# Kernel tuning notes

Measured on AMD Instinct MI355X. Metric: run time of the kernel, lower is better.

Reference implementation:

```python
import jax, jax.numpy as jnp
import numpy as np

B, T, E, H = 2, 2048, 1024, 16
D = E // H  # head_dim = 64


def setup_inputs() -> dict:
    key = jax.random.key(0)
    ks = jax.random.split(key, 9)
    s = 0.02
    x = jax.random.normal(ks[0], (B, T, E), dtype=jnp.float32)
    # additive causal mask, broadcastable to (B, H, T, T)
    causal = jnp.tril(jnp.ones((T, T), dtype=bool))
    uni_causal_mask = jnp.where(causal, 0.0, -1e9).astype(jnp.float32)[None, None]
    # torch Linear weights are (out_features, in_features); out = H*D, in = D
    Wq = jax.random.normal(ks[1], (H * D, D), dtype=jnp.float32) * s
    bq = jax.random.normal(ks[2], (H * D,), dtype=jnp.float32) * s
    Wk = jax.random.normal(ks[3], (H * D, D), dtype=jnp.float32) * s
    bk = jax.random.normal(ks[4], (H * D,), dtype=jnp.float32) * s
    Wv = jax.random.normal(ks[5], (H * D, D), dtype=jnp.float32) * s
    bv = jax.random.normal(ks[6], (H * D,), dtype=jnp.float32) * s
    Wp = jax.random.normal(ks[7], (E, E), dtype=jnp.float32) * s
    bp = jax.random.normal(ks[8], (E,), dtype=jnp.float32) * s
    return {"x": x, "uni_causal_mask": uni_causal_mask,
            "Wq": Wq, "bq": bq, "Wk": Wk, "bk": bk,
            "Wv": Wv, "bv": bv, "Wp": Wp, "bp": bp}


def _per_head_proj(xh, W, b):
    # xh: (B, T, H, D). Original code projects each head's D-dim slice with
    # Linear(D, H*D) and get_head_dim keeps only the diagonal block i for
    # head i, i.e. each head uses W[i*D:(i+1)*D, :] and b[i*D:(i+1)*D].
    W3 = W.reshape(H, D, D)  # (H, out D, in D)
    b2 = b.reshape(H, D)
    y = jnp.einsum('bthi,hoi->bhto', xh, W3) + b2[None, :, None, :]
    return y  # (B, H, T, D)


def reference(x, uni_causal_mask, Wq, bq, Wk, bk, Wv, bv, Wp, bp):
    b, t, e = x.shape
    xh = x.reshape(b, t, H, D)
    q = _per_head_proj(xh, Wq, bq)  # (B,H,T,D)
    k = _per_head_proj(xh, Wk, bk)
    v = _per_head_proj(xh, Wv, bv)
    scale = D ** (-0.5)
    attn = jnp.einsum('bhtd,bhsd->bhts', (q * scale).astype(jnp.float32),
                      k.astype(jnp.float32))
    attn = attn + uni_causal_mask
    attn = jax.nn.softmax(attn, axis=-1).astype(x.dtype)
    out = jnp.einsum('bhts,bhsd->bhtd', attn, v)
    out = out.transpose(0, 2, 1, 3).reshape(b, t, e)
    return out @ Wp.T + bp
```

## Files before the change

### kernel.cpp

```cpp
#include <hip/hip_runtime.h>

typedef __attribute__((ext_vector_type(4))) float f32x4;
typedef __attribute__((ext_vector_type(8))) __bf16 bf16x8;
typedef __attribute__((ext_vector_type(4))) unsigned short us4;
typedef __attribute__((ext_vector_type(8))) unsigned short us8;

#define DEVI static __device__ __forceinline__

constexpr int T_ = 2048, E_ = 1024, H_ = 16, D_ = 64;
#define QSCALE (0.125f * 1.44269504088896f)

DEVI unsigned short f2b(float f) {
  union { __bf16 b; unsigned short u; } c; c.b = (__bf16)f; return c.u;
}

#if __has_builtin(__builtin_amdgcn_exp2f)
DEVI float fexp2(float x) { return __builtin_amdgcn_exp2f(x); }
#else
DEVI float fexp2(float x) { return __expf(x * 0.69314718056f); }
#endif

DEVI f32x4 mfma16(bf16x8 a, bf16x8 b, f32x4 c) {
  return __builtin_amdgcn_mfma_f32_16x16x32_bf16(a, b, c, 0, 0, 0);
}

__launch_bounds__(256)
__global__ void wcvt_kernel(const float* __restrict__ Wq,
                            const float* __restrict__ Wk,
                            const float* __restrict__ Wv,
                            unsigned short* __restrict__ wqb,
                            unsigned short* __restrict__ wkb,
                            unsigned short* __restrict__ wvb)
{
  int blk = blockIdx.x;
  const float* src; unsigned short* dst; float s = 1.0f;
  if (blk < 64)       { src = Wq; dst = wqb; s = QSCALE; }
  else if (blk < 128) { src = Wk; dst = wkb; blk -= 64; }
  else                { src = Wv; dst = wvb; blk -= 128; }
  int i = blk * 256 + threadIdx.x;
  float4 v = *(const float4*)(src + (size_t)i * 4);
  us4 o; o[0] = f2b(v.x * s); o[1] = f2b(v.y * s); o[2] = f2b(v.z * s); o[3] = f2b(v.w * s);
  *(us4*)(dst + (size_t)i * 4) = o;
}

__launch_bounds__(256)
__global__ void wpcvt_kernel(const float* __restrict__ Wp,
                             unsigned short* __restrict__ wpb)
{
  int i = blockIdx.x * 256 + threadIdx.x;
  float4 v = *(const float4*)(Wp + (size_t)i * 4);
  us4 o; o[0] = f2b(v.x); o[1] = f2b(v.y); o[2] = f2b(v.z); o[3] = f2b(v.w);
  *(us4*)(wpb + (size_t)i * 4) = o;
}

__launch_bounds__(256)
__global__ void qkv_kernel(const float* __restrict__ x,
                           const unsigned short* __restrict__ wqb,
                           const float* __restrict__ bq,
                           const unsigned short* __restrict__ wkb,
                           const float* __restrict__ bk,
                           const unsigned short* __restrict__ wvb,
                           const float* __restrict__ bv,
                           unsigned short* __restrict__ qo,
                           unsigned short* __restrict__ ko,
                           unsigned short* __restrict__ vto)
{
  const int bh = blockIdx.x;
  const int b  = bh >> 4;
  const int h  = bh & (H_ - 1);
  const int t0 = blockIdx.y * 128;
  __shared__ unsigned short Xl[128][72];
  __shared__ unsigned short Wl[3][64][72];
  const int tid = threadIdx.x;

  #pragma unroll
  for (int p = 0; p < 8; ++p) {
    int idx = p * 256 + tid;
    int row = idx >> 4, c4 = idx & 15;
    float4 v = *(const float4*)(x + ((size_t)(b * T_ + t0 + row)) * E_ + h * 64 + c4 * 4);
    us4 o; o[0] = f2b(v.x); o[1] = f2b(v.y); o[2] = f2b(v.z); o[3] = f2b(v.w);
    *(us4*)&Xl[row][c4 * 4] = o;
  }
  {
    const unsigned short* wsrc0 = wqb + (size_t)h * 4096;
    const unsigned short* wsrc1 = wkb + (size_t)h * 4096;
    const unsigned short* wsrc2 = wvb + (size_t)h * 4096;
    #pragma unroll
    for (int p = 0; p < 2; ++p) {
      int idx = p * 256 + tid;
      int row = idx >> 3, c8 = (idx & 7) * 8;
      *(us8*)&Wl[0][row][c8] = *(const us8*)(wsrc0 + row * 64 + c8);
      *(us8*)&Wl[1][row][c8] = *(const us8*)(wsrc1 + row * 64 + c8);
      *(us8*)&Wl[2][row][c8] = *(const us8*)(wsrc2 + row * 64 + c8);
    }
  }
  __syncthreads();

  const int w = tid >> 6, lane = tid & 63, lo = lane & 15, g = lane >> 4;
  const int tl0 = w * 32;

  bf16x8 xb[2][2];
  #pragma unroll
  for (int tt = 0; tt < 2; ++tt)
    #pragma unroll
    for (int kd = 0; kd < 2; ++kd)
      xb[tt][kd] = *(const bf16x8*)&Xl[tl0 + tt * 16 + lo][kd * 32 + g * 8];

  #pragma unroll
  for (int tsel = 0; tsel < 2; ++tsel) {
    const float* bias = tsel ? bk : bq;
    unsigned short* outp = tsel ? ko : qo;
    const float bs = tsel ? 1.0f : QSCALE;
    #pragma unroll
    for (int ot = 0; ot < 4; ++ot) {
      bf16x8 a0 = *(const bf16x8*)&Wl[tsel][ot * 16 + lo][g * 8];
      bf16x8 a1 = *(const bf16x8*)&Wl[tsel][ot * 16 + lo][32 + g * 8];
      float4 bv4 = *(const float4*)(bias + h * 64 + ot * 16 + g * 4);
      float bb[4] = {bv4.x * bs, bv4.y * bs, bv4.z * bs, bv4.w * bs};
      #pragma unroll
      for (int tt = 0; tt < 2; ++tt) {
        f32x4 acc = {0.f, 0.f, 0.f, 0.f};
        acc = mfma16(a0, xb[tt][0], acc);
        acc = mfma16(a1, xb[tt][1], acc);
        int tg = t0 + tl0 + tt * 16 + lo;
        us4 pk;
        #pragma unroll
        for (int r = 0; r < 4; ++r) pk[r] = f2b(acc[r] + bb[r]);
        *(us4*)(outp + ((size_t)(bh * T_ + tg)) * 64 + ot * 16 + g * 4) = pk;
      }
    }
  }

  #pragma unroll
  for (int rt = 0; rt < 2; ++rt) {
    bf16x8 a0 = *(const bf16x8*)&Xl[tl0 + rt * 16 + lo][g * 8];
    bf16x8 a1 = *(const bf16x8*)&Xl[tl0 + rt * 16 + lo][32 + g * 8];
    #pragma unroll
    for (int ct = 0; ct < 4; ++ct) {
      bf16x8 b0 = *(const bf16x8*)&Wl[2][ct * 16 + lo][g * 8];
      bf16x8 b1 = *(const bf16x8*)&Wl[2][ct * 16 + lo][32 + g * 8];
      f32x4 acc = {0.f, 0.f, 0.f, 0.f};
      acc = mfma16(a0, b0, acc);
      acc = mfma16(a1, b1, acc);
      int d = ct * 16 + lo;
      float bvs = bv[h * 64 + d];
      int tg = t0 + tl0 + rt * 16 + g * 4;
      us4 pk;
      #pragma unroll
      for (int r = 0; r < 4; ++r) pk[r] = f2b(acc[r] + bvs);
      *(us4*)(vto + ((size_t)(bh * 64 + d)) * T_ + tg) = pk;
    }
  }
}

__launch_bounds__(256)
__global__ void flash_kernel(const unsigned short* __restrict__ q,
                             const unsigned short* __restrict__ kk_,
                             const unsigned short* __restrict__ vt,
                             unsigned short* __restrict__ ao)
{
  const int bh = blockIdx.x;
  const int b = bh >> 4, h = bh & 15;
  const int qt = 31 - blockIdx.y;
  const int t0 = qt * 64;
  __shared__ unsigned short Kl[2][64][64];
  __shared__ unsigned short Vl[3][64][64];
  __shared__ unsigned short Pl[4][16][64];
  const int tid = threadIdx.x, w = tid >> 6, lane = tid & 63, lo = lane & 15, g = lane >> 4;
  const int rs = lo & 7;

  const int srow = tid >> 3, sgi = tid & 7;
  const int sgis = (sgi ^ (srow & 7)) * 8;
  const unsigned short* kbase = kk_ + ((size_t)bh * T_ + srow) * 64 + sgi * 8;
  const unsigned short* vbase = vt + ((size_t)(bh * 64 + srow)) * T_ + sgi * 8;

  const int tw = t0 + w * 16;

  bf16x8 qf[2];
  const unsigned short* qb = q + ((size_t)(bh * T_ + tw + lo)) * 64;
  #pragma unroll
  for (int kd = 0; kd < 2; ++kd)
    qf[kd] = *(const bf16x8*)(qb + kd * 32 + g * 8);

  float m_ = -1e30f, l_ = 0.f;
  f32x4 zero4 = {0.f, 0.f, 0.f, 0.f};
  f32x4 oacc[4];
  #pragma unroll
  for (int dt = 0; dt < 4; ++dt) oacc[dt] = zero4;

  const int nsteps = qt + 1;
  us8 kr0 = *(const us8*)(kbase);
  us8 kr1 = *(const us8*)(kbase + 2048);
  us8 vr0 = *(const us8*)(vbase);
  us8 vr1 = *(const us8*)(vbase + (size_t)32 * T_);
  *(us8*)&Kl[0][srow][sgis] = kr0;
  *(us8*)&Kl[0][srow + 32][sgis] = kr1;
  *(us8*)&Vl[0][srow][sgis] = vr0;
  *(us8*)&Vl[0][srow + 32][sgis] = vr1;
  if (nsteps > 1) {
    kr0 = *(const us8*)(kbase + 4096);
    kr1 = *(const us8*)(kbase + 4096 + 2048);
    vr0 = *(const us8*)(vbase + 64);
    vr1 = *(const us8*)(vbase + 64 + (size_t)32 * T_);
  }
  __syncthreads();

  bf16x8 pb[2];
  int vprev = 0;

  for (int stp = 0; stp < nsteps; ++stp) {
    const int cur = stp & 1;
    us8 nk0, nk1, nv0, nv1;
    const bool pf = (stp + 2 < nsteps);
    if (pf) {
      const size_t ko_ = (size_t)(stp + 2) * 4096;
      nk0 = *(const us8*)(kbase + ko_);
      nk1 = *(const us8*)(kbase + ko_ + 2048);
      nv0 = *(const us8*)(vbase + (stp + 2) * 64);
      nv1 = *(const us8*)(vbase + (stp + 2) * 64 + (size_t)32 * T_);
    }
    f32x4 sacc[4];
    #pragma unroll
    for (int ss = 0; ss < 4; ++ss) sacc[ss] = zero4;
    __builtin_amdgcn_s_setprio(1);
    #pragma unroll
    for (int ss = 0; ss < 4; ++ss) {
      bf16x8 ka0 = *(const bf16x8*)&Kl[cur][ss * 16 + lo][(g ^ rs) * 8];
      bf16x8 ka1 = *(const bf16x8*)&Kl[cur][ss * 16 + lo][((g | 4) ^ rs) * 8];
      sacc[ss] = mfma16(ka0, qf[0], sacc[ss]);
      sacc[ss] = mfma16(ka1, qf[1], sacc[ss]);
    }
    if (stp > 0) {
      #pragma unroll
      for (int kh = 0; kh < 2; ++kh) {
        #pragma unroll
        for (int dt = 0; dt < 4; ++dt) {
          bf16x8 va = *(const bf16x8*)&Vl[vprev][dt * 16 + lo][((kh * 4 + g) ^ rs) * 8];
          oacc[dt] = mfma16(va, pb[kh], oacc[dt]);
        }
      }
    }
    __builtin_amdgcn_s_setprio(0);
    if (stp == nsteps - 1) {
      #pragma unroll
      for (int ss = 0; ss < 4; ++ss)
        #pragma unroll
        for (int r = 0; r < 4; ++r) {
          int sg = t0 + ss * 16 + g * 4 + r;
          if (sg > tw + lo) sacc[ss][r] = -1e30f;
        }
    }
    float mx = -1e30f;
    #pragma unroll
    for (int ss = 0; ss < 4; ++ss) {
      float a = fmaxf(sacc[ss][0], sacc[ss][1]);
      float c = fmaxf(sacc[ss][2], sacc[ss][3]);
      mx = fmaxf(mx, fmaxf(a, c));
    }
    if (!__all(mx <= m_ + 8.0f)) {
      mx = fmaxf(mx, __shfl_xor(mx, 16));
      mx = fmaxf(mx, __shfl_xor(mx, 32));
      float mn = fmaxf(m_, mx);
      float corr = fexp2(m_ - mn);
      m_ = mn;
      l_ *= corr;
      #pragma unroll
      for (int dt = 0; dt < 4; ++dt) oacc[dt] *= corr;
    }
    float sum = 0.f;
    #pragma unroll
    for (int ss = 0; ss < 4; ++ss) {
      us4 pk;
      #pragma unroll
      for (int r = 0; r < 4; ++r) {
        float pv = fexp2(sacc[ss][r] - m_);
        sum += pv;
        pk[r] = f2b(pv);
      }
      *(us4*)&Pl[w][lo][(((ss * 2 + (g >> 1)) ^ rs) << 3) + (g & 1) * 4] = pk;
    }
    l_ += sum;
    pb[0] = *(const bf16x8*)&Pl[w][lo][(g ^ rs) * 8];
    pb[1] = *(const bf16x8*)&Pl[w][lo][((4 + g) ^ rs) * 8];
    vprev = stp % 3;
    if (stp + 1 < nsteps) {
      *(us8*)&Kl[cur ^ 1][srow][sgis] = kr0;
      *(us8*)&Kl[cur ^ 1][srow + 32][sgis] = kr1;
      const int vn = (stp + 1) % 3;
      *(us8*)&Vl[vn][srow][sgis] = vr0;
      *(us8*)&Vl[vn][srow + 32][sgis] = vr1;
    }
    __syncthreads();
    if (pf) { kr0 = nk0; kr1 = nk1; vr0 = nv0; vr1 = nv1; }
  }
  __builtin_amdgcn_s_setprio(1);
  #pragma unroll
  for (int kh = 0; kh < 2; ++kh) {
    #pragma unroll
    for (int dt = 0; dt < 4; ++dt) {
      bf16x8 va = *(const bf16x8*)&Vl[vprev][dt * 16 + lo][((kh * 4 + g) ^ rs) * 8];
      oacc[dt] = mfma16(va, pb[kh], oacc[dt]);
    }
  }
  __builtin_amdgcn_s_setprio(0);
  l_ += __shfl_xor(l_, 16);
  l_ += __shfl_xor(l_, 32);
  float inv = 1.0f / l_;
  unsigned short* op = ao + ((size_t)(b * T_ + tw + lo)) * E_ + h * 64;
  #pragma unroll
  for (int dt = 0; dt < 4; ++dt) {
    us4 pk;
    #pragma unroll
    for (int r = 0; r < 4; ++r) pk[r] = f2b(oacc[dt][r] * inv);
    *(us4*)(op + dt * 16 + g * 4) = pk;
  }
}

__launch_bounds__(256)
__global__ void proj_kernel(const unsigned short* __restrict__ ao,
                            const unsigned short* __restrict__ wpb,
                            const float* __restrict__ bp,
                            float* __restrict__ out)
{
  const int m0 = blockIdx.x * 128;
  const int n0 = blockIdx.y * 64;
  __shared__ unsigned short Al[2][128][40];
  __shared__ unsigned short Bl[2][64][40];
  const int tid = threadIdx.x, w = tid >> 6, lane = tid & 63, lo = lane & 15, g = lane >> 4;
  const int wr = (w >> 1) * 64, wc = (w & 1) * 32;
  f32x4 zero4 = {0.f, 0.f, 0.f, 0.f};
  f32x4 acc[4][2];
  #pragma unroll
  for (int i = 0; i < 4; ++i)
    #pragma unroll
    for (int j = 0; j < 2; ++j) acc[i][j] = zero4;

  const int arow = tid >> 1, acol = (tid & 1) * 16;
  const int brow = tid >> 2, bcol = (tid & 3) * 8;
  const unsigned short* abase = ao + (size_t)(m0 + arow) * 1024 + acol;
  const unsigned short* bbase = wpb + (size_t)(n0 + brow) * 1024 + bcol;

  us8 a0 = *(const us8*)(abase);
  us8 a1 = *(const us8*)(abase + 8);
  us8 b0 = *(const us8*)(bbase);
  *(us8*)&Al[0][arow][acol] = a0;
  *(us8*)&Al[0][arow][acol + 8] = a1;
  *(us8*)&Bl[0][brow][bcol] = b0;
  a0 = *(const us8*)(abase + 32);
  a1 = *(const us8*)(abase + 40);
  b0 = *(const us8*)(bbase + 32);
  __syncthreads();

  for (int it = 0; it < 32; ++it) {
    const int cur = it & 1;
    us8 na0, na1, nb0;
    const bool pf = (it + 2 < 32);
    if (pf) {
      const int kn = (it + 2) * 32;
      na0 = *(const us8*)(abase + kn);
      na1 = *(const us8*)(abase + kn + 8);
      nb0 = *(const us8*)(bbase + kn);
    }
    bf16x8 af[4], bfr[2];
    #pragma unroll
    for (int i = 0; i < 4; ++i) af[i] = *(const bf16x8*)&Al[cur][wr + i * 16 + lo][g * 8];
    #pragma unroll
    for (int j = 0; j < 2; ++j) bfr[j] = *(const bf16x8*)&Bl[cur][wc + j * 16 + lo][g * 8];
    __builtin_amdgcn_s_setprio(1);
    #pragma unroll
    for (int i = 0; i < 4; ++i)
      #pragma unroll
      for (int j = 0; j < 2; ++j)
        acc[i][j] = mfma16(af[i], bfr[j], acc[i][j]);
    __builtin_amdgcn_s_setprio(0);
    if (it + 1 < 32) {
      *(us8*)&Al[cur ^ 1][arow][acol] = a0;
      *(us8*)&Al[cur ^ 1][arow][acol + 8] = a1;
      *(us8*)&Bl[cur ^ 1][brow][bcol] = b0;
    }
    __syncthreads();
    if (pf) { a0 = na0; a1 = na1; b0 = nb0; }
  }
  #pragma unroll
  for (int j = 0; j < 2; ++j) {
    int n = n0 + wc + j * 16 + lo;
    float bias = bp[n];
    #pragma unroll
    for (int i = 0; i < 4; ++i) {
      #pragma unroll
      for (int r = 0; r < 4; ++r)
        out[(size_t)(m0 + wr + i * 16 + g * 4 + r) * 1024 + n] = acc[i][j][r] + bias;
    }
  }
}

extern "C" void kernel_launch(void* const* d_in, const int* in_sizes, int n_in,
                              void* d_out, int out_size, void* d_ws, size_t ws_size,
                              hipStream_t stream)
{
  const float* x  = (const float*)d_in[0];
  const float* Wq = (const float*)d_in[2];
  const float* bq = (const float*)d_in[3];
  const float* Wk = (const float*)d_in[4];
  const float* bk = (const float*)d_in[5];
  const float* Wv = (const float*)d_in[6];
  const float* bv = (const float*)d_in[7];
  const float* Wp = (const float*)d_in[8];
  const float* bp = (const float*)d_in[9];
  float* out = (float*)d_out;

  char* ws = (char*)d_ws;
  const size_t SZ = (size_t)2 * 16 * 2048 * 64 * 2;
  unsigned short* q  = (unsigned short*)(ws);
  unsigned short* kb = (unsigned short*)(ws + SZ);
  unsigned short* vt = (unsigned short*)(ws + 2 * SZ);
  unsigned short* ao = (unsigned short*)(ws + 3 * SZ);
  unsigned short* wqb = ao;
  unsigned short* wkb = ao + 65536;
  unsigned short* wvb = ao + 131072;
  unsigned short* wpb = q;

  wcvt_kernel<<<dim3(192), 256, 0, stream>>>(Wq, Wk, Wv, wqb, wkb, wvb);
  qkv_kernel<<<dim3(32, 16), 256, 0, stream>>>(x, wqb, bq, wkb, bk, wvb, bv, q, kb, vt);
  flash_kernel<<<dim3(32, 32), 256, 0, stream>>>(q, kb, vt, ao);
  wpcvt_kernel<<<dim3(1024), 256, 0, stream>>>(Wp, wpb);
  proj_kernel<<<dim3(32, 16), 256, 0, stream>>>(ao, wpb, bp, out);
}
```

Before: 79.33 us.

## Keep P in registers via permuted K/V layouts, MFMA row sums, XCD-aware proj grid

Permutes the K rows and V columns as they are staged into shared memory so the S-accumulator layout from the QK^T MFMA matches the B-operand layout for PV. P can then be packed straight into registers, with no round trip through a shared-memory P buffer. The softmax row sum is computed with an MFMA against a ones vector instead of scalar adds and cross-lane shuffles. Separately, the projection kernel uses a 1D grid remapped so tiles sharing rows land on the same XCD for L2 reuse. The trade-offs are split 8-byte global loads for V and an extra MFMA per half-tile.

```diff
diff --git a/kernel.cpp b/kernel.cpp
--- a/kernel.cpp
+++ b/kernel.cpp
@@ -12,6 +12,11 @@
 
 DEVI unsigned short f2b(float f) {
   union { __bf16 b; unsigned short u; } c; c.b = (__bf16)f; return c.u;
+}
+
+DEVI unsigned pkw(float a, float b) {
+  union { __bf16 h[2]; unsigned u; } c;
+  c.h[0] = (__bf16)a; c.h[1] = (__bf16)b; return c.u;
 }
 
 #if __has_builtin(__builtin_amdgcn_exp2f)
@@ -165,14 +170,20 @@
   const int t0 = qt * 64;
   __shared__ unsigned short Kl[2][64][64];
   __shared__ unsigned short Vl[3][64][64];
-  __shared__ unsigned short Pl[4][16][64];
   const int tid = threadIdx.x, w = tid >> 6, lane = tid & 63, lo = lane & 15, g = lane >> 4;
   const int rs = lo & 7;
 
   const int srow = tid >> 3, sgi = tid & 7;
-  const int sgis = (sgi ^ (srow & 7)) * 8;
+  const int khalf = (srow >> 2) & 1;
+  const int gsrc = (srow >> 3) ^ (khalf << 1);
+  const int prow = khalf * 16 + gsrc * 4 + (srow & 3);
+  const int kkey = (sgi ^ (prow & 7)) * 8;
+  const int vkey = (sgi ^ (srow & 7)) * 8;
   const unsigned short* kbase = kk_ + ((size_t)bh * T_ + srow) * 64 + sgi * 8;
-  const unsigned short* vbase = vt + ((size_t)(bh * 64 + srow)) * T_ + sgi * 8;
+  const unsigned short* vrow0 = vt + ((size_t)(bh * 64 + srow)) * T_;
+  const unsigned short* vrow1 = vrow0 + (size_t)32 * T_;
+  const int vco0 = sgi * 8;
+  const int vco1 = ((sgi ^ 2) * 8) + 4;
 
   const int tw = t0 + w * 16;
 
@@ -182,26 +193,39 @@
   for (int kd = 0; kd < 2; ++kd)
     qf[kd] = *(const bf16x8*)(qb + kd * 32 + g * 8);
 
-  float m_ = -1e30f, l_ = 0.f;
+  const int sb0 = g * 8, sb1 = ((g ^ 2) * 8) + 4;
+
+  union { unsigned u[4]; bf16x8 v; } onec;
+  onec.u[0] = onec.u[1] = onec.u[2] = onec.u[3] = 0x3f803f80u;
+  const bf16x8 onesv = onec.v;
+
+  float m_ = -1e30f;
   f32x4 zero4 = {0.f, 0.f, 0.f, 0.f};
+  f32x4 lacc = zero4;
   f32x4 oacc[4];
   #pragma unroll
   for (int dt = 0; dt < 4; ++dt) oacc[dt] = zero4;
 
   const int nsteps = qt + 1;
+  union u8c { us4 h[2]; us8 v; };
   us8 kr0 = *(const us8*)(kbase);
   us8 kr1 = *(const us8*)(kbase + 2048);
-  us8 vr0 = *(const us8*)(vbase);
-  us8 vr1 = *(const us8*)(vbase + (size_t)32 * T_);
-  *(us8*)&Kl[0][srow][sgis] = kr0;
-  *(us8*)&Kl[0][srow + 32][sgis] = kr1;
-  *(us8*)&Vl[0][srow][sgis] = vr0;
-  *(us8*)&Vl[0][srow + 32][sgis] = vr1;
+  u8c vr0, vr1;
+  vr0.h[0] = *(const us4*)(vrow0 + vco0);
+  vr0.h[1] = *(const us4*)(vrow0 + vco1);
+  vr1.h[0] = *(const us4*)(vrow1 + vco0);
+  vr1.h[1] = *(const us4*)(vrow1 + vco1);
+  *(us8*)&Kl[0][prow][kkey] = kr0;
+  *(us8*)&Kl[0][prow + 32][kkey] = kr1;
+  *(us8*)&Vl[0][srow][vkey] = vr0.v;
+  *(us8*)&Vl[0][srow + 32][vkey] = vr1.v;
   if (nsteps > 1) {
     kr0 = *(const us8*)(kbase + 4096);
     kr1 = *(const us8*)(kbase + 4096 + 2048);
-    vr0 = *(const us8*)(vbase + 64);
-    vr1 = *(const us8*)(vbase + 64 + (size_t)32 * T_);
+    vr0.h[0] = *(const us4*)(vrow0 + 64 + vco0);
+    vr0.h[1] = *(const us4*)(vrow0 + 64 + vco1);
+    vr1.h[0] = *(const us4*)(vrow1 + 64 + vco0);
+    vr1.h[1] = *(const us4*)(vrow1 + 64 + vco1);
   }
   __syncthreads();
 
@@ -210,14 +234,18 @@
 
   for (int stp = 0; stp < nsteps; ++stp) {
     const int cur = stp & 1;
-    us8 nk0, nk1, nv0, nv1;
+    us8 nk0, nk1;
+    u8c nv0, nv1;
     const bool pf = (stp + 2 < nsteps);
     if (pf) {
       const size_t ko_ = (size_t)(stp + 2) * 4096;
+      const int so = (stp + 2) * 64;
       nk0 = *(const us8*)(kbase + ko_);
       nk1 = *(const us8*)(kbase + ko_ + 2048);
-      nv0 = *(const us8*)(vbase + (stp + 2) * 64);
-      nv1 = *(const us8*)(vbase + (stp + 2) * 64 + (size_t)32 * T_);
+      nv0.h[0] = *(const us4*)(vrow0 + so + vco0);
+      nv0.h[1] = *(const us4*)(vrow0 + so + vco1);
+      nv1.h[0] = *(const us4*)(vrow1 + so + vco0);
+      nv1.h[1] = *(const us4*)(vrow1 + so + vco1);
     }
     f32x4 sacc[4];
     #pragma unroll
@@ -243,12 +271,13 @@
     __builtin_amdgcn_s_setprio(0);
     if (stp == nsteps - 1) {
       #pragma unroll
-      for (int ss = 0; ss < 4; ++ss)
+      for (int ss = 0; ss < 4; ++ss) {
+        const int sb = ((ss & 1) ? sb1 : sb0) + (ss >> 1) * 32;
         #pragma unroll
         for (int r = 0; r < 4; ++r) {
-          int sg = t0 + ss * 16 + g * 4 + r;
-          if (sg > tw + lo) sacc[ss][r] = -1e30f;
+          if (t0 + sb + r > tw + lo) sacc[ss][r] = -1e30f;
         }
+      }
     }
     float mx = -1e30f;
     #pragma unroll
@@ -263,32 +292,33 @@
       float mn = fmaxf(m_, mx);
       float corr = fexp2(m_ - mn);
       m_ = mn;
-      l_ *= corr;
+      lacc *= corr;
       #pragma unroll
       for (int dt = 0; dt < 4; ++dt) oacc[dt] *= corr;
     }
-    float sum = 0.f;
-    #pragma unroll
-    for (int ss = 0; ss < 4; ++ss) {
-      us4 pk;
-      #pragma unroll
-      for (int r = 0; r < 4; ++r) {
-        float pv = fexp2(sacc[ss][r] - m_);
-        sum += pv;
-        pk[r] = f2b(pv);
+    #pragma unroll
+    for (int kh = 0; kh < 2; ++kh) {
+      union { unsigned u[4]; bf16x8 v; } pbc;
+      #pragma unroll
+      for (int half2 = 0; half2 < 2; ++half2) {
+        const int ss = kh * 2 + half2;
+        float p0 = fexp2(sacc[ss][0] - m_);
+        float p1 = fexp2(sacc[ss][1] - m_);
+        float p2 = fexp2(sacc[ss][2] - m_);
+        float p3 = fexp2(sacc[ss][3] - m_);
+        pbc.u[half2 * 2]     = pkw(p0, p1);
+        pbc.u[half2 * 2 + 1] = pkw(p2, p3);
       }
-      *(us4*)&Pl[w][lo][(((ss * 2 + (g >> 1)) ^ rs) << 3) + (g & 1) * 4] = pk;
-    }
-    l_ += sum;
-    pb[0] = *(const bf16x8*)&Pl[w][lo][(g ^ rs) * 8];
-    pb[1] = *(const bf16x8*)&Pl[w][lo][((4 + g) ^ rs) * 8];
+      pb[kh] = pbc.v;
+      lacc = mfma16(onesv, pb[kh], lacc);
+    }
     vprev = stp % 3;
     if (stp + 1 < nsteps) {
-      *(us8*)&Kl[cur ^ 1][srow][sgis] = kr0;
-      *(us8*)&Kl[cur ^ 1][srow + 32][sgis] = kr1;
+      *(us8*)&Kl[cur ^ 1][prow][kkey] = kr0;
+      *(us8*)&Kl[cur ^ 1][prow + 32][kkey] = kr1;
       const int vn = (stp + 1) % 3;
-      *(us8*)&Vl[vn][srow][sgis] = vr0;
-      *(us8*)&Vl[vn][srow + 32][sgis] = vr1;
+      *(us8*)&Vl[vn][srow][vkey] = vr0.v;
+      *(us8*)&Vl[vn][srow + 32][vkey] = vr1.v;
     }
     __syncthreads();
     if (pf) { kr0 = nk0; kr1 = nk1; vr0 = nv0; vr1 = nv1; }
@@ -303,9 +333,7 @@
     }
   }
   __builtin_amdgcn_s_setprio(0);
-  l_ += __shfl_xor(l_, 16);
-  l_ += __shfl_xor(l_, 32);
-  float inv = 1.0f / l_;
+  float inv = 1.0f / lacc[0];
   unsigned short* op = ao + ((size_t)(b * T_ + tw + lo)) * E_ + h * 64;
   #pragma unroll
   for (int dt = 0; dt < 4; ++dt) {
@@ -322,8 +350,10 @@
                             const float* __restrict__ bp,
                             float* __restrict__ out)
 {
-  const int m0 = blockIdx.x * 128;
-  const int n0 = blockIdx.y * 64;
+  const int bid = blockIdx.x;
+  const int xcd = bid & 7, idx = bid >> 3;
+  const int m0 = (xcd * 4 + (idx & 3)) * 128;
+  const int n0 = (idx >> 2) * 64;
   __shared__ unsigned short Al[2][128][40];
   __shared__ unsigned short Bl[2][64][40];
   const int tid = threadIdx.x, w = tid >> 6, lane = tid & 63, lo = lane & 15, g = lane >> 4;
@@ -424,5 +454,5 @@
   qkv_kernel<<<dim3(32, 16), 256, 0, stream>>>(x, wqb, bq, wkb, bk, wvb, bv, q, kb, vt);
   flash_kernel<<<dim3(32, 32), 256, 0, stream>>>(q, kb, vt, ao);
   wpcvt_kernel<<<dim3(1024), 256, 0, stream>>>(Wp, wpb);
-  proj_kernel<<<dim3(32, 16), 256, 0, stream>>>(ao, wpb, bp, out);
-}
+  proj_kernel<<<dim3(512), 256, 0, stream>>>(ao, wpb, bp, out);
+}
```

New measurement: 79.81 us. Within noise of the previous version (+0.6%).
